# Performance work log

Hardware: AMD Instinct MI355X
Metric: run time of the kernel (lower is better)

Reference implementation:

```python
import jax, jax.numpy as jnp
import numpy as np

D = 768   # embedding_dimensions (richness) — hardcoded in source
H = 3     # heads — hardcoded in source


def setup_inputs() -> dict:
    key = jax.random.key(0)
    ks = jax.random.split(key, 12)
    s = 1.0 / np.sqrt(D)
    s3 = 1.0 / np.sqrt(H * D)
    return {
        "x": jax.random.normal(ks[0], (4, 2048, D), dtype=jnp.float32),
        # QKV projections: Linear(D, D*H), stored as (in, out)
        "Wq": jax.random.uniform(ks[1], (D, D * H), jnp.float32, -s, s),
        "bq": jax.random.uniform(ks[2], (D * H,), jnp.float32, -s, s),
        "Wk": jax.random.uniform(ks[3], (D, D * H), jnp.float32, -s, s),
        "bk": jax.random.uniform(ks[4], (D * H,), jnp.float32, -s, s),
        "Wv": jax.random.uniform(ks[5], (D, D * H), jnp.float32, -s, s),
        "bv": jax.random.uniform(ks[6], (D * H,), jnp.float32, -s, s),
        # final projection: Linear(H*D, D)
        "Wo": jax.random.uniform(ks[7], (H * D, D), jnp.float32, -s3, s3),
        "bo": jax.random.uniform(ks[8], (D,), jnp.float32, -s3, s3),
        # FFN: Linear(D, D) + LeakyReLU
        "Wf": jax.random.uniform(ks[9], (D, D), jnp.float32, -s, s),
        "bf": jax.random.uniform(ks[10], (D,), jnp.float32, -s, s),
    }


def reference(x, Wq, bq, Wk, bk, Wv, bv, Wo, bo, Wf, bf):
    B, S, _ = x.shape
    # QKV: [B,S,H*D] -> [B,H,S,D]  (head dim == full D, as in source)
    q = (x @ Wq + bq).reshape(B, S, H, D).transpose(0, 2, 1, 3)
    k = (x @ Wk + bk).reshape(B, S, H, D).transpose(0, 2, 1, 3)
    v = (x @ Wv + bv).reshape(B, S, H, D).transpose(0, 2, 1, 3)
    # unscaled attention scores (source applies no 1/sqrt(d))
    scores = jnp.einsum('bhqd,bhkd->bhqk', q, k)
    # faithful masking: tril of the scores themselves, fill zeros with -99999
    masked = jnp.where(jnp.tril(scores) == 0, jnp.float32(-99999.0), scores)
    attn = jax.nn.softmax(masked, axis=-1)
    o = jnp.einsum('bhqk,bhkd->bhqd', attn, v)
    o = o.transpose(0, 2, 1, 3).reshape(B, S, H * D)
    a = o @ Wo + bo
    # "normalisation": subtract global mean over the whole tensor
    n = a - jnp.mean(a)
    y = n + x  # residual
    return jax.nn.leaky_relu(y @ Wf + bf, negative_slope=0.01)
```

## Files before the change

### kernel.cpp

```cpp
#include <hip/hip_runtime.h>
#include <hip/hip_bf16.h>

typedef __attribute__((ext_vector_type(8))) __bf16 bf16x8;
typedef __attribute__((ext_vector_type(4))) float f32x4;
typedef unsigned short u16;

#define DEV static __device__ __forceinline__

#define BAR() asm volatile("s_barrier" ::: "memory")
#define LGKM0() asm volatile("s_waitcnt lgkmcnt(0)" ::: "memory")
#define VMCNT3() asm volatile("s_waitcnt vmcnt(3)" ::: "memory")
#define VMCNT0() asm volatile("s_waitcnt vmcnt(0)" ::: "memory")

DEV void load_lds16(const void* g, void* l) {
  __builtin_amdgcn_global_load_lds(
      (const __attribute__((address_space(1))) unsigned int*)g,
      (__attribute__((address_space(3))) unsigned int*)l, 16, 0, 0);
}

DEV u16 bf16bits(float v) {
  __hip_bfloat16 h = __float2bfloat16(v);
  return __builtin_bit_cast(u16, h);
}

DEV float bf2f(u16 u) {
  return __builtin_bit_cast(float, (unsigned)u << 16);
}

DEV bf16x8 rdfrag(const u16* region, int row, int ks, int l) {
  const int cb = (((ks << 6) | ((l >> 4) << 4)) ^ ((l & 7) << 4));
  return *(const bf16x8*)((const char*)region + row * 128 + cb);
}

DEV bf16x8 rdfrag32(const u16* region, int row, int l) {
  const int cb = (((l >> 4) ^ (row & 3)) << 4);
  return *(const bf16x8*)((const char*)region + row * 64 + cb);
}

struct OffN { unsigned long long a[12], b[12], c[12]; };

enum { G128_SC = 0, G128_PV = 1, G128_PLAIN = 2, G128_LEAKY = 3 };

__global__ __launch_bounds__(512, 1) void k_qkv256(
    const u16* __restrict__ A, const u16* __restrict__ B,
    const float* __restrict__ bias, u16* __restrict__ C, u16* __restrict__ Vt)
{
  int flat = blockIdx.y * 27 + blockIdx.x;
  flat = (flat & 7) * 108 + (flat >> 3);
  const int n0 = (flat % 27) * 256, m0 = (flat / 27) * 256;
  const int lda = 768, ldb = 768, nkt = 12;

  __shared__ u16 smem[65536];
  u16* As0 = smem;
  u16* Bs0 = smem + 32768;

  const int tid = threadIdx.x;
  const int l = tid & 63;
  const int wid = tid >> 6;
  const int wm = wid >> 1, wn = wid & 1;

  const int r0s = wid * 16 + (l >> 3);
  const int ces = ((l & 7) ^ (l >> 3)) << 3;
  const size_t aR0 = (size_t)(m0 + r0s) * lda + ces;
  const size_t aR1 = aR0 + (size_t)8 * lda;
  const size_t bR0 = (size_t)(n0 + r0s) * ldb + ces;
  const size_t bR1 = bR0 + (size_t)8 * ldb;
  const size_t hA = (size_t)128 * lda, hB = (size_t)128 * ldb;
  const int dst0 = wid * 1024 + l * 8, dst1 = dst0 + 512;

#define STAGE_A(bf, h, kkv) do {                                 \
    u16* Lp = As0 + (bf) * 16384 + (h) * 8192;                   \
    load_lds16(A + aR0 + ((h) ? hA : 0) + (kkv), Lp + dst0);     \
    load_lds16(A + aR1 + ((h) ? hA : 0) + (kkv), Lp + dst1);     \
  } while (0)
#define STAGE_B(bf, h, kkv) do {                                 \
    u16* Lp = Bs0 + (bf) * 16384 + (h) * 8192;                   \
    load_lds16(B + bR0 + ((h) ? hB : 0) + (kkv), Lp + dst0);     \
    load_lds16(B + bR1 + ((h) ? hB : 0) + (kkv), Lp + dst1);     \
  } while (0)

  f32x4 acc[2][2][2][4] = {};
  bf16x8 af[2][2], bA[4][2], bB[4][2];

#define MFMA16(QM, QN, BARR)                                                  \
    __builtin_amdgcn_s_setprio(1);                                            \
    _Pragma("unroll") for (int ks = 0; ks < 2; ks++)                          \
      _Pragma("unroll") for (int fm = 0; fm < 2; fm++)                        \
        _Pragma("unroll") for (int fn = 0; fn < 4; fn++)                      \
          acc[QM][QN][fm][fn] = __builtin_amdgcn_mfma_f32_16x16x32_bf16(      \
              af[fm][ks], BARR[fn][ks], acc[QM][QN][fm][fn], 0, 0, 0);        \
    __builtin_amdgcn_s_setprio(0);

#define RD_A(half)                                                            \
    _Pragma("unroll") for (int fm = 0; fm < 2; fm++)                          \
      _Pragma("unroll") for (int ks = 0; ks < 2; ks++)                        \
        af[fm][ks] = rdfrag(half, wm * 32 + fm * 16 + (l & 15), ks, l);
#define RD_B(dstv, half)                                                      \
    _Pragma("unroll") for (int fn = 0; fn < 4; fn++)                          \
      _Pragma("unroll") for (int ks = 0; ks < 2; ks++)                        \
        dstv[fn][ks] = rdfrag(half, wn * 64 + fn * 16 + (l & 15), ks, l);

  STAGE_A(0, 0, 0); STAGE_B(0, 0, 0); STAGE_B(0, 1, 0); STAGE_A(0, 1, 0);
  STAGE_A(1, 0, 64); STAGE_B(1, 0, 64); STAGE_B(1, 1, 64);
  VMCNT3();
  BAR();

  for (int t = 0; t < nkt; ++t) {
    const int cur = t & 1, nxt = cur ^ 1;
    const int kk1 = (t + 1) << 6, kk2 = (t + 2) << 6;
    const bool s1 = (t + 1 < nkt), s2 = (t + 2 < nkt);
    RD_A(As0 + cur * 16384);
    RD_B(bA, Bs0 + cur * 16384);
    if (s1) STAGE_A(nxt, 1, kk1);
    BAR(); LGKM0();
    MFMA16(0, 0, bA);
    BAR();
    RD_B(bB, Bs0 + cur * 16384 + 8192);
    if (s2) STAGE_A(cur, 0, kk2);
    BAR(); LGKM0();
    MFMA16(0, 1, bB);
    BAR();
    RD_A(As0 + cur * 16384 + 8192);
    if (s2) STAGE_B(cur, 0, kk2);
    BAR(); LGKM0();
    MFMA16(1, 1, bB);
    BAR();
    if (s2) STAGE_B(cur, 1, kk2);
    BAR();
    MFMA16(1, 0, bA);
    if (s2) { VMCNT3(); } else { VMCNT0(); }
    BAR();
  }
#undef RD_A
#undef RD_B
#undef MFMA16
#undef STAGE_A
#undef STAGE_B

  __syncthreads();
  const int sel = n0 >= 4608 ? 2 : (n0 >= 2304 ? 1 : 0);
  const int r0c = (l >> 4) << 2;
  if (sel == 2) {
#pragma unroll
    for (int Qm = 0; Qm < 2; Qm++)
#pragma unroll
      for (int Qn = 0; Qn < 2; Qn++)
#pragma unroll
        for (int fn = 0; fn < 4; fn++) {
          const int coll = Qn * 128 + wn * 64 + fn * 16 + (l & 15);
          const float bv = bias[n0 + coll];
#pragma unroll
          for (int fm = 0; fm < 2; fm++)
#pragma unroll
            for (int r = 0; r < 4; r++) {
              const int rowl = Qm * 128 + wm * 32 + fm * 16 + r0c + r;
              smem[coll * 256 + ((((rowl >> 3) ^ (coll & 7)) << 3) | (rowl & 7))] =
                  bf16bits(acc[Qm][Qn][fm][fn][r] + bv);
            }
        }
    __syncthreads();
    const int n0v = n0 - 4608;
    const int h = n0v / 768, d0l = n0v % 768;
    const int b = m0 >> 11, sbase = m0 & 2047;
    u16* Cb = Vt + ((size_t)(b * 3 + h) * 768 + d0l) * 2048 + sbase;
#pragma unroll
    for (int j = 0; j < 16; j++) {
      const int dr = j * 16 + (tid >> 5);
      const int c8 = tid & 31;
      bf16x8 v = *(const bf16x8*)&smem[dr * 256 + ((c8 ^ (dr & 7)) << 3)];
      *(bf16x8*)&Cb[(size_t)dr * 2048 + c8 * 8] = v;
    }
  } else {
#pragma unroll
    for (int Qm = 0; Qm < 2; Qm++)
#pragma unroll
      for (int Qn = 0; Qn < 2; Qn++)
#pragma unroll
        for (int fn = 0; fn < 4; fn++) {
          const int coll = Qn * 128 + wn * 64 + fn * 16 + (l & 15);
          const float bv = bias[n0 + coll];
#pragma unroll
          for (int fm = 0; fm < 2; fm++)
#pragma unroll
            for (int r = 0; r < 4; r++) {
              const int rowl = Qm * 128 + wm * 32 + fm * 16 + r0c + r;
              smem[rowl * 256 + (coll ^ (((rowl >> 2) & 3) << 4))] =
                  bf16bits(acc[Qm][Qn][fm][fn][r] + bv);
            }
        }
    __syncthreads();
    u16* Cb = C + (size_t)sel * (8192ull * 2304) + (n0 - sel * 2304);
#pragma unroll
    for (int j = 0; j < 16; j++) {
      const int rowl = j * 16 + (tid >> 5);
      const int c = (tid & 31) * 8;
      bf16x8 v = *(const bf16x8*)&smem[rowl * 256 + (c ^ (((rowl >> 2) & 3) << 4))];
      *(bf16x8*)&Cb[(size_t)(m0 + rowl) * 2304 + c] = v;
    }
  }
}

template<int MODE>
__global__ __launch_bounds__(512, 4) void k_g128(
    const u16* __restrict__ Abase, const u16* __restrict__ Bbase,
    const float* __restrict__ bias, void* __restrict__ Cbase,
    float* __restrict__ part,
    long lda, long ldb, long ldc, int K, OffN off)
{
  int m0, n0, z, r = 0, rb = 0, nkt, arow0, brow0;
  const u16 *A, *B;
  if (MODE == G128_SC) {
    r = blockIdx.y; z = blockIdx.z;
    rb = r >> 1;
    if ((int)blockIdx.x > rb) return;
    m0 = r * 128; n0 = blockIdx.x * 256;
    nkt = K >> 5;
    A = Abase + off.a[z]; B = Bbase + off.b[z];
    arow0 = m0; brow0 = n0;
  } else if (MODE == G128_PV) {
    r = 15 - (int)blockIdx.y;
    rb = r >> 1;
    z = blockIdx.x / 3;
    m0 = r * 128; n0 = (blockIdx.x % 3) * 256;
    nkt = (rb + 1) * 8;
    lda = (long)(rb + 1) * 256;
    A = Abase + off.a[z] + (size_t)32768 * rb * (rb + 1);
    B = Bbase + off.b[z];
    arow0 = (r & 1) * 128; brow0 = n0;
  } else {
    z = 0;
    m0 = blockIdx.y * 128; n0 = blockIdx.x * 256;
    nkt = K >> 5;
    A = Abase; B = Bbase;
    arow0 = m0; brow0 = n0;
  }

  __shared__ u16 smem[36864];

  const int tid = threadIdx.x;
  const int l = tid & 63;
  const int wid = tid >> 6;
  const int wm = wid & 1;
  const int wn = wid >> 1;

  const int ces = (((tid & 3) ^ ((tid >> 2) & 3)) << 3);
  const u16* aS  = A + (size_t)(arow0 + (tid >> 2)) * lda + ces;
  const u16* bS0 = B + (size_t)(brow0 + (tid >> 2)) * ldb + ces;
  const u16* bS1 = bS0 + (size_t)128 * ldb;
  const int t8 = tid * 8;

#define STG(buf, kkv) do {                         \
    u16* Lp = smem + (buf) * 12288;                \
    load_lds16(aS  + (kkv), Lp + t8);              \
    load_lds16(bS0 + (kkv), Lp + 4096 + t8);       \
    load_lds16(bS1 + (kkv), Lp + 8192 + t8);       \
  } while (0)

  f32x4 acc[4][4] = {};
  bf16x8 af[4], bf[4];

  STG(0, 0);
  STG(1, 32);
  VMCNT3();
  BAR();

  for (int t = 0; t < nkt; ++t) {
    const u16* Ar = smem + (t % 3) * 12288;
    const u16* Br = Ar + 4096;
#pragma unroll
    for (int fm = 0; fm < 4; fm++)
      af[fm] = rdfrag32(Ar, wm * 64 + fm * 16 + (l & 15), l);
#pragma unroll
    for (int fn = 0; fn < 4; fn++)
      bf[fn] = rdfrag32(Br, wn * 64 + fn * 16 + (l & 15), l);
    const bool s2 = (t + 2 < nkt);
    if (s2) STG((t + 2) % 3, (t + 2) << 5);
    BAR(); LGKM0();
    __builtin_amdgcn_s_setprio(1);
#pragma unroll
    for (int fm = 0; fm < 4; fm++)
#pragma unroll
      for (int fn = 0; fn < 4; fn++)
        acc[fm][fn] = __builtin_amdgcn_mfma_f32_16x16x32_bf16(
            af[fm], bf[fn], acc[fm][fn], 0, 0, 0);
    __builtin_amdgcn_s_setprio(0);
    if (s2) { VMCNT3(); } else if (t + 1 < nkt) { VMCNT0(); }
    BAR();
  }
#undef STG

  const int r0c = (l >> 4) << 2;
  if (MODE == G128_SC) {
    float mx4[4][4], s4[4][4];
#pragma unroll
    for (int fm = 0; fm < 4; fm++)
#pragma unroll
      for (int rr = 0; rr < 4; rr++) {
        const int gi = m0 + wm * 64 + fm * 16 + r0c + rr;
        float mv = -1e30f;
#pragma unroll
        for (int fn = 0; fn < 4; fn++) {
          const int gc = n0 + wn * 64 + fn * 16 + (l & 15);
          float v = (gc <= gi) ? acc[fm][fn][rr] : -1e30f;
          acc[fm][fn][rr] = v;
          mv = fmaxf(mv, v);
        }
        mx4[fm][rr] = mv;
      }
#pragma unroll
    for (int o = 1; o < 16; o <<= 1)
#pragma unroll
      for (int fm = 0; fm < 4; fm++)
#pragma unroll
        for (int rr = 0; rr < 4; rr++)
          mx4[fm][rr] = fmaxf(mx4[fm][rr], __shfl_xor(mx4[fm][rr], o, 64));
    float* redm = (float*)smem;
    float* reds = redm + 512;
#pragma unroll
    for (int fm = 0; fm < 4; fm++)
#pragma unroll
      for (int rr = 0; rr < 4; rr++)
        if ((l & 15) == fm * 4 + rr)
          redm[(wm * 64 + fm * 16 + r0c + rr) * 4 + wn] = mx4[fm][rr];
    __syncthreads();
#pragma unroll
    for (int fm = 0; fm < 4; fm++)
#pragma unroll
      for (int rr = 0; rr < 4; rr++) {
        const int rowl = wm * 64 + fm * 16 + r0c + rr;
        f32x4 rm = *(const f32x4*)&redm[rowl * 4];
        const float tm = fmaxf(fmaxf(rm[0], rm[1]), fmaxf(rm[2], rm[3]));
        mx4[fm][rr] = tm;
        float ss = 0.f;
#pragma unroll
        for (int fn = 0; fn < 4; fn++) {
          const float e = __expf(acc[fm][fn][rr] - tm);
          acc[fm][fn][rr] = e;
          ss += e;
        }
        s4[fm][rr] = ss;
      }
#pragma unroll
    for (int o = 1; o < 16; o <<= 1)
#pragma unroll
      for (int fm = 0; fm < 4; fm++)
#pragma unroll
        for (int rr = 0; rr < 4; rr++)
          s4[fm][rr] += __shfl_xor(s4[fm][rr], o, 64);
#pragma unroll
    for (int fm = 0; fm < 4; fm++)
#pragma unroll
      for (int rr = 0; rr < 4; rr++)
        if ((l & 15) == fm * 4 + rr)
          reds[(wm * 64 + fm * 16 + r0c + rr) * 4 + wn] = s4[fm][rr];
    __syncthreads();
    if (wn == 0) {
#pragma unroll
      for (int fm = 0; fm < 4; fm++)
#pragma unroll
        for (int rr = 0; rr < 4; rr++)
          if ((l & 15) == fm * 4 + rr) {
            const int rowl = wm * 64 + fm * 16 + r0c + rr;
            f32x4 rs = *(const f32x4*)&reds[rowl * 4];
            float2 pw;
            pw.x = mx4[fm][rr];
            pw.y = rs[0] + rs[1] + rs[2] + rs[3];
            *(float2*)&part[(size_t)z * 32768 +
                            ((size_t)(m0 + rowl) * 8 + blockIdx.x) * 2] = pw;
          }
    }
    __syncthreads();
#pragma unroll
    for (int fn = 0; fn < 4; fn++) {
      const int coll = wn * 64 + fn * 16 + (l & 15);
#pragma unroll
      for (int fm = 0; fm < 4; fm++)
#pragma unroll
        for (int rr = 0; rr < 4; rr++) {
          const int rowl = wm * 64 + fm * 16 + r0c + rr;
          smem[rowl * 256 + (coll ^ (((rowl >> 2) & 3) << 4))] =
              bf16bits(acc[fm][fn][rr]);
        }
    }
    __syncthreads();
    u16* Cb = (u16*)Cbase + off.c[z] + (size_t)32768 * rb * (rb + 1);
    const int W = (rb + 1) << 8;
    const int pr0 = (r & 1) * 128;
#pragma unroll
    for (int j = 0; j < 8; j++) {
      const int rowl = j * 16 + (tid >> 5);
      const int c = (tid & 31) * 8;
      bf16x8 v = *(const bf16x8*)&smem[rowl * 256 + (c ^ (((rowl >> 2) & 3) << 4))];
      *(bf16x8*)&Cb[(size_t)(pr0 + rowl) * W + n0 + c] = v;
    }
  } else if (MODE == G128_PV) {
    __syncthreads();
#pragma unroll
    for (int fn = 0; fn < 4; fn++) {
      const int coll = wn * 64 + fn * 16 + (l & 15);
#pragma unroll
      for (int fm = 0; fm < 4; fm++)
#pragma unroll
        for (int rr = 0; rr < 4; rr++) {
          const int rowl = wm * 64 + fm * 16 + r0c + rr;
          smem[rowl * 256 + (coll ^ (((rowl >> 2) & 3) << 4))] =
              bf16bits(acc[fm][fn][rr]);
        }
    }
    __syncthreads();
    u16* Cb = (u16*)Cbase + off.c[z] + n0;
#pragma unroll
    for (int j = 0; j < 8; j++) {
      const int rowl = j * 16 + (tid >> 5);
      const int c = (tid & 31) * 8;
      bf16x8 v = *(const bf16x8*)&smem[rowl * 256 + (c ^ (((rowl >> 2) & 3) << 4))];
      *(bf16x8*)&Cb[(size_t)(m0 + rowl) * 2304 + c] = v;
    }
  } else {
#pragma unroll
    for (int fn = 0; fn < 4; fn++) {
      const int col = n0 + wn * 64 + fn * 16 + (l & 15);
      const float bv = bias[col];
#pragma unroll
      for (int fm = 0; fm < 4; fm++)
#pragma unroll
        for (int rr = 0; rr < 4; rr++) {
          const int rowl = wm * 64 + fm * 16 + r0c + rr;
          float v = acc[fm][fn][rr] + bv;
          if (MODE == G128_LEAKY) v = v > 0.f ? v : 0.01f * v;
          ((float*)Cbase)[(size_t)(m0 + rowl) * ldc + col] = v;
        }
    }
  }
}

__global__ __launch_bounds__(256) void k_cast_x(const float* __restrict__ in,
                                                u16* __restrict__ out) {
  const size_t i = ((size_t)blockIdx.x * 256 + threadIdx.x) * 4;
  float4 v = *(const float4*)&in[i];
  ushort4 o;
  o.x = bf16bits(v.x); o.y = bf16bits(v.y); o.z = bf16bits(v.z); o.w = bf16bits(v.w);
  *(ushort4*)&out[i] = o;
}

__global__ __launch_bounds__(256) void k_wt(const float* __restrict__ in,
                                            u16* __restrict__ out, int R, int C) {
  __shared__ float tile[32][33];
  const int c0 = blockIdx.x * 32, r0 = blockIdx.y * 32;
  const int tx = threadIdx.x, ty = threadIdx.y;
#pragma unroll
  for (int k = 0; k < 4; k++)
    tile[ty + 8 * k][tx] = in[(size_t)(r0 + ty + 8 * k) * C + c0 + tx];
  __syncthreads();
#pragma unroll
  for (int k = 0; k < 4; k++)
    out[(size_t)(c0 + ty + 8 * k) * R + r0 + tx] = bf16bits(tile[tx][ty + 8 * k]);
}

__global__ __launch_bounds__(256) void k_bias_concat(const float* __restrict__ bq,
                                                     const float* __restrict__ bk,
                                                     const float* __restrict__ bv,
                                                     float* __restrict__ out) {
  const int i = blockIdx.x * 256 + threadIdx.x;
  if (i < 2304) out[i] = bq[i];
  else if (i < 4608) out[i] = bk[i - 2304];
  else if (i < 6912) out[i] = bv[i - 4608];
}

__global__ __launch_bounds__(256) void k_rescale(u16* __restrict__ P,
                                                 const float* __restrict__ part) {
  const int w = threadIdx.x >> 6, l = threadIdx.x & 63;
  const int gi = blockIdx.x * 4 + w;
  const int z = blockIdx.y;
  const int rb = gi >> 8;
  const int W = (rb + 1) << 8;
  const float2* pp = (const float2*)part + (size_t)z * 16384 + (size_t)gi * 8;
  float m = -1e30f;
#pragma unroll
  for (int t = 0; t < 8; t++)
    if (t <= rb) m = fmaxf(m, pp[t].x);
  float den = 0.f;
#pragma unroll
  for (int t = 0; t < 8; t++)
    if (t <= rb) den += pp[t].y * __expf(pp[t].x - m);
  const float inv = 1.f / den;
  u16* Prow = P + (size_t)z * 2359296 + (size_t)32768 * rb * (rb + 1) +
              (size_t)(gi & 255) * W;
#pragma unroll
  for (int t = 0; t < 8; t++)
    if (t <= rb) {
      const float ft = __expf(pp[t].x - m) * inv;
      ushort4 v = *(const ushort4*)&Prow[t * 256 + l * 4];
      v.x = bf16bits(bf2f(v.x) * ft);
      v.y = bf16bits(bf2f(v.y) * ft);
      v.z = bf16bits(bf2f(v.z) * ft);
      v.w = bf16bits(bf2f(v.w) * ft);
      *(ushort4*)&Prow[t * 256 + l * 4] = v;
    }
}

__global__ __launch_bounds__(256) void k_red1(const float* __restrict__ a,
                                              float* __restrict__ part) {
  float s = 0.f;
  for (size_t idx = (size_t)blockIdx.x * 256 + threadIdx.x; idx < 6291456ull; idx += 2048ull * 256)
    s += a[idx];
#pragma unroll
  for (int o = 32; o >= 1; o >>= 1) s += __shfl_xor(s, o, 64);
  __shared__ float r[4];
  const int t = threadIdx.x, w = t >> 6;
  if ((t & 63) == 0) r[w] = s;
  __syncthreads();
  if (t == 0) part[blockIdx.x] = r[0] + r[1] + r[2] + r[3];
}

__global__ __launch_bounds__(256) void k_red2(const float* __restrict__ part,
                                              float* __restrict__ mean) {
  const int t = threadIdx.x;
  float s = 0.f;
  for (int i = t; i < 2048; i += 256) s += part[i];
#pragma unroll
  for (int o = 32; o >= 1; o >>= 1) s += __shfl_xor(s, o, 64);
  __shared__ float r[4];
  const int w = t >> 6;
  if ((t & 63) == 0) r[w] = s;
  __syncthreads();
  if (t == 0) mean[0] = (r[0] + r[1] + r[2] + r[3]) * (1.f / 6291456.f);
}

__global__ __launch_bounds__(256) void k_residual(const float* __restrict__ a,
                                                  const float* __restrict__ x,
                                                  const float* __restrict__ meanp,
                                                  u16* __restrict__ yb) {
  const float mean = meanp[0];
  const size_t i = ((size_t)blockIdx.x * 256 + threadIdx.x) * 4;
  float4 av = *(const float4*)&a[i];
  float4 xv = *(const float4*)&x[i];
  ushort4 o;
  o.x = bf16bits(av.x - mean + xv.x);
  o.y = bf16bits(av.y - mean + xv.y);
  o.z = bf16bits(av.z - mean + xv.z);
  o.w = bf16bits(av.w - mean + xv.w);
  *(ushort4*)&yb[i] = o;
}

extern "C" void kernel_launch(void* const* d_in, const int* in_sizes, int n_in,
                              void* d_out, int out_size, void* d_ws, size_t ws_size,
                              hipStream_t stream) {
  const float* x   = (const float*)d_in[0];
  const float* Wq  = (const float*)d_in[1];
  const float* bq  = (const float*)d_in[2];
  const float* Wk  = (const float*)d_in[3];
  const float* bk  = (const float*)d_in[4];
  const float* Wv  = (const float*)d_in[5];
  const float* bv  = (const float*)d_in[6];
  const float* Wo  = (const float*)d_in[7];
  const float* bo  = (const float*)d_in[8];
  const float* Wf  = (const float*)d_in[9];
  const float* bfb = (const float*)d_in[10];

  char* ws = (char*)d_ws;
  const size_t MSZ    = 37748736;
  const size_t o_Wqkvt = 0;
  const size_t o_Wot  = 10616832;
  const size_t o_Wft  = o_Wot + 3538944;
  const size_t o_bqkv = o_Wft + 1179648;
  const size_t o_prt  = o_bqkv + 32768;
  const size_t o_mn   = o_prt + 8192;
  const size_t o_part = o_mn + 256;
  const size_t o_xb   = o_part + 1572864;
  const size_t o_Q    = o_xb + 12582912;
  const size_t o_K    = o_Q + MSZ;
  const size_t o_Vt   = o_K + MSZ;
  const size_t o_P    = o_Vt + MSZ;
  const size_t o_end  = o_P + 56623104;
  if (ws_size < o_end) return;

  const size_t o_O  = o_Q;
  const size_t o_a  = o_K;
  const size_t o_yb = o_xb;

  OffN z0{};
  dim3 b32(32, 8);

  k_cast_x<<<6144, 256, 0, stream>>>(x, (u16*)(ws + o_xb));
  k_wt<<<dim3(72, 24), b32, 0, stream>>>(Wq, (u16*)(ws + o_Wqkvt), 768, 2304);
  k_wt<<<dim3(72, 24), b32, 0, stream>>>(Wk, (u16*)(ws + o_Wqkvt) + 2304 * 768, 768, 2304);
  k_wt<<<dim3(72, 24), b32, 0, stream>>>(Wv, (u16*)(ws + o_Wqkvt) + 2 * 2304 * 768, 768, 2304);
  k_wt<<<dim3(24, 72), b32, 0, stream>>>(Wo, (u16*)(ws + o_Wot), 2304, 768);
  k_wt<<<dim3(24, 24), b32, 0, stream>>>(Wf, (u16*)(ws + o_Wft), 768, 768);
  k_bias_concat<<<27, 256, 0, stream>>>(bq, bk, bv, (float*)(ws + o_bqkv));

  k_qkv256<<<dim3(27, 32), 512, 0, stream>>>(
      (const u16*)(ws + o_xb), (const u16*)(ws + o_Wqkvt),
      (const float*)(ws + o_bqkv), (u16*)(ws + o_Q), (u16*)(ws + o_Vt));

  OffN so{}, po{};
  for (int zz = 0; zz < 12; zz++) {
    const int b = zz / 3, h = zz % 3;
    so.a[zz] = (size_t)b * 2048 * 2304 + (size_t)h * 768;
    so.b[zz] = so.a[zz];
    so.c[zz] = (size_t)zz * 2359296;
    po.a[zz] = so.c[zz];
    po.b[zz] = (size_t)zz * 768 * 2048;
    po.c[zz] = so.a[zz];
  }
  k_g128<G128_SC><<<dim3(8, 16, 12), 512, 0, stream>>>(
      (const u16*)(ws + o_Q), (const u16*)(ws + o_K), nullptr, ws + o_P,
      (float*)(ws + o_part), 2304, 2304, 0, 768, so);
  k_rescale<<<dim3(512, 12), 256, 0, stream>>>((u16*)(ws + o_P),
                                               (const float*)(ws + o_part));
  k_g128<G128_PV><<<dim3(36, 16), 512, 0, stream>>>(
      (const u16*)(ws + o_P), (const u16*)(ws + o_Vt), nullptr, ws + o_O,
      nullptr, 0, 2048, 0, 0, po);

  k_g128<G128_PLAIN><<<dim3(3, 64), 512, 0, stream>>>(
      (const u16*)(ws + o_O), (const u16*)(ws + o_Wot), bo, ws + o_a,
      nullptr, 2304, 2304, 768, 2304, z0);

  k_red1<<<2048, 256, 0, stream>>>((const float*)(ws + o_a), (float*)(ws + o_prt));
  k_red2<<<1, 256, 0, stream>>>((const float*)(ws + o_prt), (float*)(ws + o_mn));
  k_residual<<<6144, 256, 0, stream>>>((const float*)(ws + o_a), x,
                                       (const float*)(ws + o_mn), (u16*)(ws + o_yb));

  k_g128<G128_LEAKY><<<dim3(3, 64), 512, 0, stream>>>(
      (const u16*)(ws + o_yb), (const u16*)(ws + o_Wft), bfb, d_out,
      nullptr, 768, 768, 768, 768, z0);
}
```

Measured before the change: 418.3 us.

## Shrink g128 GEMM tiles to 128x128 for finer causal skipping and occupancy

The shared g128 GEMM kernel drops its N tile from 256 to 128 columns, with half the LDS footprint and half the accumulators. Launch bounds rise to 6 blocks per CU and the grids double. For the causal score kernel, the smaller tiles skip more masked blocks, so the per-tile softmax partial layout and the rescale kernel are reworked for 16 column tiles. The mid-loop barrier is removed, the LDS swizzle is changed, and masked entries are zeroed explicitly. The aim is to cut wasted causal work and improve latency hiding, at the cost of more partial statistics and less operand reuse per tile.

```diff
diff --git a/kernel.cpp b/kernel.cpp
--- a/kernel.cpp
+++ b/kernel.cpp
@@ -10,6 +10,7 @@
 #define BAR() asm volatile("s_barrier" ::: "memory")
 #define LGKM0() asm volatile("s_waitcnt lgkmcnt(0)" ::: "memory")
 #define VMCNT3() asm volatile("s_waitcnt vmcnt(3)" ::: "memory")
+#define VMCNT2() asm volatile("s_waitcnt vmcnt(2)" ::: "memory")
 #define VMCNT0() asm volatile("s_waitcnt vmcnt(0)" ::: "memory")
 
 DEV void load_lds16(const void* g, void* l) {
@@ -33,7 +34,7 @@
 }
 
 DEV bf16x8 rdfrag32(const u16* region, int row, int l) {
-  const int cb = (((l >> 4) ^ (row & 3)) << 4);
+  const int cb = (((l >> 4) ^ ((row >> 1) & 3)) << 4);
   return *(const bf16x8*)((const char*)region + row * 64 + cb);
 }
 
@@ -51,8 +52,6 @@
   const int lda = 768, ldb = 768, nkt = 12;
 
   __shared__ u16 smem[65536];
-  u16* As0 = smem;
-  u16* Bs0 = smem + 32768;
 
   const int tid = threadIdx.x;
   const int l = tid & 63;
@@ -67,6 +66,8 @@
   const size_t bR1 = bR0 + (size_t)8 * ldb;
   const size_t hA = (size_t)128 * lda, hB = (size_t)128 * ldb;
   const int dst0 = wid * 1024 + l * 8, dst1 = dst0 + 512;
+  u16* As0 = smem;
+  u16* Bs0 = smem + 32768;
 
 #define STAGE_A(bf, h, kkv) do {                                 \
     u16* Lp = As0 + (bf) * 16384 + (h) * 8192;                   \
@@ -201,27 +202,27 @@
 }
 
 template<int MODE>
-__global__ __launch_bounds__(512, 4) void k_g128(
+__global__ __launch_bounds__(512, 6) void k_g128(
     const u16* __restrict__ Abase, const u16* __restrict__ Bbase,
     const float* __restrict__ bias, void* __restrict__ Cbase,
     float* __restrict__ part,
     long lda, long ldb, long ldc, int K, OffN off)
 {
-  int m0, n0, z, r = 0, rb = 0, nkt, arow0, brow0;
+  int m0, n0, z, r = 0, rb = 0, nkt, arow0, brow0, bx = 0;
   const u16 *A, *B;
   if (MODE == G128_SC) {
-    r = blockIdx.y; z = blockIdx.z;
+    r = blockIdx.y; z = blockIdx.z; bx = blockIdx.x;
     rb = r >> 1;
-    if ((int)blockIdx.x > rb) return;
-    m0 = r * 128; n0 = blockIdx.x * 256;
+    if (bx > (r | 1)) return;
+    m0 = r * 128; n0 = bx * 128;
     nkt = K >> 5;
     A = Abase + off.a[z]; B = Bbase + off.b[z];
     arow0 = m0; brow0 = n0;
   } else if (MODE == G128_PV) {
     r = 15 - (int)blockIdx.y;
     rb = r >> 1;
-    z = blockIdx.x / 3;
-    m0 = r * 128; n0 = (blockIdx.x % 3) * 256;
+    z = blockIdx.x / 6;
+    m0 = r * 128; n0 = (blockIdx.x % 6) * 128;
     nkt = (rb + 1) * 8;
     lda = (long)(rb + 1) * 256;
     A = Abase + off.a[z] + (size_t)32768 * rb * (rb + 1);
@@ -229,13 +230,13 @@
     arow0 = (r & 1) * 128; brow0 = n0;
   } else {
     z = 0;
-    m0 = blockIdx.y * 128; n0 = blockIdx.x * 256;
+    m0 = blockIdx.y * 128; n0 = blockIdx.x * 128;
     nkt = K >> 5;
     A = Abase; B = Bbase;
     arow0 = m0; brow0 = n0;
   }
 
-  __shared__ u16 smem[36864];
+  __shared__ u16 smem[24576];
 
   const int tid = threadIdx.x;
   const int l = tid & 63;
@@ -243,48 +244,46 @@
   const int wm = wid & 1;
   const int wn = wid >> 1;
 
-  const int ces = (((tid & 3) ^ ((tid >> 2) & 3)) << 3);
-  const u16* aS  = A + (size_t)(arow0 + (tid >> 2)) * lda + ces;
-  const u16* bS0 = B + (size_t)(brow0 + (tid >> 2)) * ldb + ces;
-  const u16* bS1 = bS0 + (size_t)128 * ldb;
+  const int ces = (((tid & 3) ^ ((tid >> 3) & 3)) << 3);
+  const u16* aS = A + (size_t)(arow0 + (tid >> 2)) * lda + ces;
+  const u16* bS = B + (size_t)(brow0 + (tid >> 2)) * ldb + ces;
   const int t8 = tid * 8;
 
-#define STG(buf, kkv) do {                         \
-    u16* Lp = smem + (buf) * 12288;                \
-    load_lds16(aS  + (kkv), Lp + t8);              \
-    load_lds16(bS0 + (kkv), Lp + 4096 + t8);       \
-    load_lds16(bS1 + (kkv), Lp + 8192 + t8);       \
+#define STG(buf, kkv) do {                    \
+    u16* Lp = smem + (buf) * 8192;            \
+    load_lds16(aS + (kkv), Lp + t8);          \
+    load_lds16(bS + (kkv), Lp + 4096 + t8);   \
   } while (0)
 
-  f32x4 acc[4][4] = {};
-  bf16x8 af[4], bf[4];
+  f32x4 acc[4][2] = {};
+  bf16x8 af[4], bf[2];
 
   STG(0, 0);
   STG(1, 32);
-  VMCNT3();
+  VMCNT2();
   BAR();
 
   for (int t = 0; t < nkt; ++t) {
-    const u16* Ar = smem + (t % 3) * 12288;
+    const u16* Ar = smem + (t % 3) * 8192;
     const u16* Br = Ar + 4096;
 #pragma unroll
     for (int fm = 0; fm < 4; fm++)
       af[fm] = rdfrag32(Ar, wm * 64 + fm * 16 + (l & 15), l);
 #pragma unroll
-    for (int fn = 0; fn < 4; fn++)
-      bf[fn] = rdfrag32(Br, wn * 64 + fn * 16 + (l & 15), l);
+    for (int fn = 0; fn < 2; fn++)
+      bf[fn] = rdfrag32(Br, wn * 32 + fn * 16 + (l & 15), l);
     const bool s2 = (t + 2 < nkt);
     if (s2) STG((t + 2) % 3, (t + 2) << 5);
-    BAR(); LGKM0();
+    LGKM0();
     __builtin_amdgcn_s_setprio(1);
 #pragma unroll
     for (int fm = 0; fm < 4; fm++)
 #pragma unroll
-      for (int fn = 0; fn < 4; fn++)
+      for (int fn = 0; fn < 2; fn++)
         acc[fm][fn] = __builtin_amdgcn_mfma_f32_16x16x32_bf16(
             af[fm], bf[fn], acc[fm][fn], 0, 0, 0);
     __builtin_amdgcn_s_setprio(0);
-    if (s2) { VMCNT3(); } else if (t + 1 < nkt) { VMCNT0(); }
+    if (s2) { VMCNT2(); } else if (t + 1 < nkt) { VMCNT0(); }
     BAR();
   }
 #undef STG
@@ -299,8 +298,8 @@
         const int gi = m0 + wm * 64 + fm * 16 + r0c + rr;
         float mv = -1e30f;
 #pragma unroll
-        for (int fn = 0; fn < 4; fn++) {
-          const int gc = n0 + wn * 64 + fn * 16 + (l & 15);
+        for (int fn = 0; fn < 2; fn++) {
+          const int gc = n0 + wn * 32 + fn * 16 + (l & 15);
           float v = (gc <= gi) ? acc[fm][fn][rr] : -1e30f;
           acc[fm][fn][rr] = v;
           mv = fmaxf(mv, v);
@@ -330,11 +329,11 @@
         const int rowl = wm * 64 + fm * 16 + r0c + rr;
         f32x4 rm = *(const f32x4*)&redm[rowl * 4];
         const float tm = fmaxf(fmaxf(rm[0], rm[1]), fmaxf(rm[2], rm[3]));
-        mx4[fm][rr] = tm;
         float ss = 0.f;
 #pragma unroll
-        for (int fn = 0; fn < 4; fn++) {
-          const float e = __expf(acc[fm][fn][rr] - tm);
+        for (int fn = 0; fn < 2; fn++) {
+          const float v = acc[fm][fn][rr];
+          const float e = (v > -1e29f) ? __expf(v - tm) : 0.f;
           acc[fm][fn][rr] = e;
           ss += e;
         }
@@ -354,31 +353,24 @@
         if ((l & 15) == fm * 4 + rr)
           reds[(wm * 64 + fm * 16 + r0c + rr) * 4 + wn] = s4[fm][rr];
     __syncthreads();
-    if (wn == 0) {
-#pragma unroll
-      for (int fm = 0; fm < 4; fm++)
-#pragma unroll
-        for (int rr = 0; rr < 4; rr++)
-          if ((l & 15) == fm * 4 + rr) {
-            const int rowl = wm * 64 + fm * 16 + r0c + rr;
-            f32x4 rs = *(const f32x4*)&reds[rowl * 4];
-            float2 pw;
-            pw.x = mx4[fm][rr];
-            pw.y = rs[0] + rs[1] + rs[2] + rs[3];
-            *(float2*)&part[(size_t)z * 32768 +
-                            ((size_t)(m0 + rowl) * 8 + blockIdx.x) * 2] = pw;
-          }
-    }
-    __syncthreads();
-#pragma unroll
-    for (int fn = 0; fn < 4; fn++) {
-      const int coll = wn * 64 + fn * 16 + (l & 15);
+    if (tid < 128) {
+      f32x4 rm = *(const f32x4*)&redm[tid * 4];
+      f32x4 rs = *(const f32x4*)&reds[tid * 4];
+      float2 pw;
+      pw.x = fmaxf(fmaxf(rm[0], rm[1]), fmaxf(rm[2], rm[3]));
+      pw.y = rs[0] + rs[1] + rs[2] + rs[3];
+      ((float2*)part)[((size_t)z * 16 + bx) * 2048 + m0 + tid] = pw;
+    }
+    __syncthreads();
+#pragma unroll
+    for (int fn = 0; fn < 2; fn++) {
+      const int coll = wn * 32 + fn * 16 + (l & 15);
 #pragma unroll
       for (int fm = 0; fm < 4; fm++)
 #pragma unroll
         for (int rr = 0; rr < 4; rr++) {
           const int rowl = wm * 64 + fm * 16 + r0c + rr;
-          smem[rowl * 256 + (coll ^ (((rowl >> 2) & 3) << 4))] =
+          smem[rowl * 128 + (coll ^ (((rowl >> 2) & 3) << 4))] =
               bf16bits(acc[fm][fn][rr]);
         }
     }
@@ -387,39 +379,39 @@
     const int W = (rb + 1) << 8;
     const int pr0 = (r & 1) * 128;
 #pragma unroll
-    for (int j = 0; j < 8; j++) {
-      const int rowl = j * 16 + (tid >> 5);
-      const int c = (tid & 31) * 8;
-      bf16x8 v = *(const bf16x8*)&smem[rowl * 256 + (c ^ (((rowl >> 2) & 3) << 4))];
-      *(bf16x8*)&Cb[(size_t)(pr0 + rowl) * W + n0 + c] = v;
+    for (int j = 0; j < 4; j++) {
+      const int rowl = j * 32 + (tid >> 4);
+      const int c = tid & 15;
+      bf16x8 v = *(const bf16x8*)&smem[rowl * 128 + ((c ^ (((rowl >> 2) & 3) << 1)) << 3)];
+      *(bf16x8*)&Cb[(size_t)(pr0 + rowl) * W + n0 + c * 8] = v;
     }
   } else if (MODE == G128_PV) {
     __syncthreads();
 #pragma unroll
-    for (int fn = 0; fn < 4; fn++) {
-      const int coll = wn * 64 + fn * 16 + (l & 15);
+    for (int fn = 0; fn < 2; fn++) {
+      const int coll = wn * 32 + fn * 16 + (l & 15);
 #pragma unroll
       for (int fm = 0; fm < 4; fm++)
 #pragma unroll
         for (int rr = 0; rr < 4; rr++) {
           const int rowl = wm * 64 + fm * 16 + r0c + rr;
-          smem[rowl * 256 + (coll ^ (((rowl >> 2) & 3) << 4))] =
+          smem[rowl * 128 + (coll ^ (((rowl >> 2) & 3) << 4))] =
               bf16bits(acc[fm][fn][rr]);
         }
     }
     __syncthreads();
     u16* Cb = (u16*)Cbase + off.c[z] + n0;
 #pragma unroll
-    for (int j = 0; j < 8; j++) {
-      const int rowl = j * 16 + (tid >> 5);
-      const int c = (tid & 31) * 8;
-      bf16x8 v = *(const bf16x8*)&smem[rowl * 256 + (c ^ (((rowl >> 2) & 3) << 4))];
-      *(bf16x8*)&Cb[(size_t)(m0 + rowl) * 2304 + c] = v;
+    for (int j = 0; j < 4; j++) {
+      const int rowl = j * 32 + (tid >> 4);
+      const int c = tid & 15;
+      bf16x8 v = *(const bf16x8*)&smem[rowl * 128 + ((c ^ (((rowl >> 2) & 3) << 1)) << 3)];
+      *(bf16x8*)&Cb[(size_t)(m0 + rowl) * 2304 + c * 8] = v;
     }
   } else {
 #pragma unroll
-    for (int fn = 0; fn < 4; fn++) {
-      const int col = n0 + wn * 64 + fn * 16 + (l & 15);
+    for (int fn = 0; fn < 2; fn++) {
+      const int col = n0 + wn * 32 + fn * 16 + (l & 15);
       const float bv = bias[col];
 #pragma unroll
       for (int fm = 0; fm < 4; fm++)
@@ -474,29 +466,26 @@
   const int z = blockIdx.y;
   const int rb = gi >> 8;
   const int W = (rb + 1) << 8;
-  const float2* pp = (const float2*)part + (size_t)z * 16384 + (size_t)gi * 8;
+  const int nt = (gi >> 7) + 1;
+  const float2* pp = (const float2*)part + (size_t)z * 16 * 2048 + gi;
   float m = -1e30f;
-#pragma unroll
-  for (int t = 0; t < 8; t++)
-    if (t <= rb) m = fmaxf(m, pp[t].x);
+  for (int t = 0; t < nt; t++) m = fmaxf(m, pp[(size_t)t * 2048].x);
   float den = 0.f;
-#pragma unroll
-  for (int t = 0; t < 8; t++)
-    if (t <= rb) den += pp[t].y * __expf(pp[t].x - m);
+  for (int t = 0; t < nt; t++) {
+    float2 q = pp[(size_t)t * 2048];
+    den += q.y * __expf(q.x - m);
+  }
   const float inv = 1.f / den;
   u16* Prow = P + (size_t)z * 2359296 + (size_t)32768 * rb * (rb + 1) +
               (size_t)(gi & 255) * W;
-#pragma unroll
-  for (int t = 0; t < 8; t++)
-    if (t <= rb) {
-      const float ft = __expf(pp[t].x - m) * inv;
-      ushort4 v = *(const ushort4*)&Prow[t * 256 + l * 4];
-      v.x = bf16bits(bf2f(v.x) * ft);
-      v.y = bf16bits(bf2f(v.y) * ft);
-      v.z = bf16bits(bf2f(v.z) * ft);
-      v.w = bf16bits(bf2f(v.w) * ft);
-      *(ushort4*)&Prow[t * 256 + l * 4] = v;
-    }
+  for (int t = 0; t < nt; t++) {
+    const float ft = __expf(pp[(size_t)t * 2048].x - m) * inv;
+    unsigned v = *(const unsigned*)&Prow[t * 128 + l * 2];
+    const float lo = bf2f((u16)(v & 0xffff)) * ft;
+    const float hi = bf2f((u16)(v >> 16)) * ft;
+    unsigned o = (unsigned)bf16bits(lo) | ((unsigned)bf16bits(hi) << 16);
+    *(unsigned*)&Prow[t * 128 + l * 2] = o;
+  }
 }
 
 __global__ __launch_bounds__(256) void k_red1(const float* __restrict__ a,
@@ -567,7 +556,7 @@
   const size_t o_prt  = o_bqkv + 32768;
   const size_t o_mn   = o_prt + 8192;
   const size_t o_part = o_mn + 256;
-  const size_t o_xb   = o_part + 1572864;
+  const size_t o_xb   = o_part + 3145728;
   const size_t o_Q    = o_xb + 12582912;
   const size_t o_K    = o_Q + MSZ;
   const size_t o_Vt   = o_K + MSZ;
@@ -604,16 +593,16 @@
     po.b[zz] = (size_t)zz * 768 * 2048;
     po.c[zz] = so.a[zz];
   }
-  k_g128<G128_SC><<<dim3(8, 16, 12), 512, 0, stream>>>(
+  k_g128<G128_SC><<<dim3(16, 16, 12), 512, 0, stream>>>(
       (const u16*)(ws + o_Q), (const u16*)(ws + o_K), nullptr, ws + o_P,
       (float*)(ws + o_part), 2304, 2304, 0, 768, so);
   k_rescale<<<dim3(512, 12), 256, 0, stream>>>((u16*)(ws + o_P),
                                                (const float*)(ws + o_part));
-  k_g128<G128_PV><<<dim3(36, 16), 512, 0, stream>>>(
+  k_g128<G128_PV><<<dim3(72, 16), 512, 0, stream>>>(
       (const u16*)(ws + o_P), (const u16*)(ws + o_Vt), nullptr, ws + o_O,
       nullptr, 0, 2048, 0, 0, po);
 
-  k_g128<G128_PLAIN><<<dim3(3, 64), 512, 0, stream>>>(
+  k_g128<G128_PLAIN><<<dim3(6, 64), 512, 0, stream>>>(
       (const u16*)(ws + o_O), (const u16*)(ws + o_Wot), bo, ws + o_a,
       nullptr, 2304, 2304, 768, 2304, z0);
 
@@ -622,7 +611,7 @@
   k_residual<<<6144, 256, 0, stream>>>((const float*)(ws + o_a), x,
                                        (const float*)(ws + o_mn), (u16*)(ws + o_yb));
 
-  k_g128<G128_LEAKY><<<dim3(3, 64), 512, 0, stream>>>(
+  k_g128<G128_LEAKY><<<dim3(6, 64), 512, 0, stream>>>(
       (const u16*)(ws + o_yb), (const u16*)(ws + o_Wft), bfb, d_out,
       nullptr, 768, 768, 768, 768, z0);
 }
```

New measurement: 450.0 us. 1.08x slower.
